# Kernel optimization log

Hardware: AMD Instinct MI355X
Metric: run time of the kernel (lower is better)

## Reference

```python
import jax, jax.numpy as jnp
import numpy as np

INPUT_DIM = 512
KEY_DIM = 256
VOCAB = 10000
MAX_LEN = 300


def setup_inputs() -> dict:
    key = jax.random.key(0)
    ks = jax.random.split(key, 20)
    s = 0.05
    B, S, D, K, V = 32, 196, INPUT_DIM, KEY_DIM, VOCAB
    inp = {
        'x': jax.random.normal(ks[0], (B, S, D), jnp.float32),
        'emb': jax.random.normal(ks[1], (V, D), jnp.float32) * s,
        'Wk': jax.random.normal(ks[2], (K, D), jnp.float32) * s,
        'bk': jnp.zeros((K,), jnp.float32),
        'Wv': jax.random.normal(ks[3], (K, D), jnp.float32) * s,
        'bv': jnp.zeros((K,), jnp.float32),
        'Wq': jax.random.normal(ks[4], (K, D), jnp.float32) * s,
        'bq': jnp.zeros((K,), jnp.float32),
        'Wp': jax.random.normal(ks[5], (V, D + K), jnp.float32) * s,
        'bp': jnp.zeros((V,), jnp.float32),
        # LSTM cell 0: input = concat(embed, context) -> D + K
        'Wih0': jax.random.normal(ks[6], (4 * D, D + K), jnp.float32) * s,
        'Whh0': jax.random.normal(ks[7], (4 * D, D), jnp.float32) * s,
        'bih0': jnp.zeros((4 * D,), jnp.float32),
        'bhh0': jnp.zeros((4 * D,), jnp.float32),
        # LSTM cell 1: input = hidden of cell 0 -> D
        'Wih1': jax.random.normal(ks[8], (4 * D, D), jnp.float32) * s,
        'Whh1': jax.random.normal(ks[9], (4 * D, D), jnp.float32) * s,
        'bih1': jnp.zeros((4 * D,), jnp.float32),
        'bhh1': jnp.zeros((4 * D,), jnp.float32),
    }
    return inp


def _lstm_cell(inp, h, c, Wih, Whh, bih, bhh):
    # torch LSTMCell gate order: i, f, g, o
    gates = inp @ Wih.T + bih + h @ Whh.T + bhh
    i, f, g, o = jnp.split(gates, 4, axis=-1)
    c_new = jax.nn.sigmoid(f) * c + jax.nn.sigmoid(i) * jnp.tanh(g)
    h_new = jax.nn.sigmoid(o) * jnp.tanh(c_new)
    return h_new, c_new


def reference(x, emb, Wk, bk, Wv, bv, Wq, bq, Wp, bp,
              Wih0, Whh0, bih0, bhh0, Wih1, Whh1, bih1, bhh1):
    B = x.shape[0]
    D = Whh0.shape[1]
    K = Wk.shape[0]
    scale = 1.0 / jnp.sqrt(jnp.asarray(K, x.dtype))
    keys = x @ Wk.T + bk      # (B, S, K)
    values = x @ Wv.T + bv    # (B, S, K)

    tok0 = jnp.zeros((B,), jnp.int32)           # argmax of zeros(B,1) == 0
    ctx0 = jnp.zeros((B, K), x.dtype)
    h0 = jnp.zeros((B, D), x.dtype)
    c0 = jnp.zeros((B, D), x.dtype)
    h1 = jnp.zeros((B, D), x.dtype)
    c1 = jnp.zeros((B, D), x.dtype)

    def step(carry, _):
        tok, ctx, h0, c0, h1, c1 = carry
        embed = jnp.concatenate([emb[tok], ctx], axis=1)   # (B, D+K)
        h0, c0 = _lstm_cell(embed, h0, c0, Wih0, Whh0, bih0, bhh0)
        h1, c1 = _lstm_cell(h0, h1, c1, Wih1, Whh1, bih1, bhh1)
        q = h1 @ Wq.T + bq                                  # (B, K)
        energy = jnp.einsum('bsk,bk->bs', keys, q) * scale  # (B, S)
        attn = jax.nn.softmax(energy, axis=-1)
        ctx = jnp.einsum('bs,bsk->bk', attn, values)        # (B, K)
        out = jnp.concatenate([h1, ctx], axis=1)            # (B, D+K)
        pred = out @ Wp.T + bp                              # (B, V)
        tok = jnp.argmax(pred, axis=-1).astype(jnp.int32)
        return (tok, ctx, h0, c0, h1, c1), pred

    _, preds = jax.lax.scan(step, (tok0, ctx0, h0, c0, h1, c1), None, length=MAX_LEN)
    return jnp.transpose(preds, (1, 0, 2))  # (B, MAX_LEN, V)
```

## Files before the change

kernel.cpp:

```cpp
#include <hip/hip_runtime.h>
#include <math.h>


typedef unsigned long long u64;
typedef float v4f __attribute__((ext_vector_type(4)));

#define NS 196
#define ND 512
#define NK 256
#define NV 10000
#define NT 300
#define NBLK 256
#define NTHR 512
#define NPRED 209
#define ATT0 224
#define SCOPE __HIP_MEMORY_SCOPE_AGENT

__device__ __forceinline__ float sigm(float x) { return 1.0f / (1.0f + expf(-x)); }

__device__ __forceinline__ float aldf(const float* p) {
  return __hip_atomic_load(p, __ATOMIC_RELAXED, SCOPE);
}
__device__ __forceinline__ void astf(float* p, float v) {
  __hip_atomic_store(p, v, __ATOMIC_RELAXED, SCOPE);
}
__device__ __forceinline__ u64 aldu(const u64* p) {
  return __hip_atomic_load(p, __ATOMIC_RELAXED, SCOPE);
}
__device__ __forceinline__ void astu(u64* p, u64 v) {
  __hip_atomic_store(p, v, __ATOMIC_RELAXED, SCOPE);
}
__device__ __forceinline__ v4f ald16(const float* p) {
  union { u64 q[2]; v4f v; } u;
  u.q[0] = __hip_atomic_load((const u64*)p + 0, __ATOMIC_RELAXED, SCOPE);
  u.q[1] = __hip_atomic_load((const u64*)p + 1, __ATOMIC_RELAXED, SCOPE);
  return u.v;
}

__device__ __forceinline__ u64 packmax(float x, int v) {
  unsigned u = __float_as_uint(x);
  u = (u & 0x80000000u) ? ~u : (u | 0x80000000u);
  return ((u64)u << 32) | (u64)(0xFFFFFFFFu - (unsigned)v);
}

__device__ __forceinline__ int eslot(int b, int k4) {
  return b * 32 + ((k4 & ~7) | ((k4 ^ b) & 7));
}

__device__ __forceinline__ void gbar(unsigned* bar, int bid, unsigned ep, bool fenced) {
  __syncthreads();
  if (threadIdx.x == 0) {
    if (fenced) __threadfence();
    asm volatile("s_waitcnt vmcnt(0)" ::: "memory");
    const int g = bid & 7;
    const unsigned old = __hip_atomic_fetch_add(&bar[g * 32], 1u, __ATOMIC_RELAXED, SCOPE);
    if (old == ep * 32u - 1u) {
      const unsigned r = __hip_atomic_fetch_add(&bar[512], 1u, __ATOMIC_RELAXED, SCOPE);
      if (r == ep * 8u - 1u) {
#pragma unroll
        for (int i = 0; i < 8; ++i)
          __hip_atomic_store(&bar[256 + i * 32], ep, __ATOMIC_RELAXED, SCOPE);
      }
    }
    while (__hip_atomic_load(&bar[256 + g * 32], __ATOMIC_RELAXED, SCOPE) < ep)
      __builtin_amdgcn_s_sleep(1);
    if (fenced) __threadfence();
  }
  __syncthreads();
}

__global__ __launch_bounds__(256) void k_zbar(unsigned* bar) {
  const int i = blockIdx.x * 256 + threadIdx.x;
  if (i < 1024) bar[i] = 0u;
}

struct Params {
  const float *x, *emb, *Wk, *bk, *Wv, *bv, *Wq, *bq, *Wp, *bp;
  const float *Wih0, *Whh0, *bih0, *bhh0, *Wih1, *Whh1, *bih1, *bhh1;
  float *out, *keys, *values, *h0t, *h1t, *c0, *c1, *ctx;
  u64 *amax;
  unsigned *bar;
};

__global__ __launch_bounds__(NTHR, 1) void k_all(Params p) {
  extern __shared__ float dyn[];
  float* W0lds = dyn;
  float* W1lds = dyn + 10240;
  float* stage = dyn + 18432;

  __shared__ __align__(16) float arena[2560];
  __shared__ int tok_lds[32];
  __shared__ u64 cand2[32][12];

  const int bid = blockIdx.x;
  const int t = threadIdx.x;
  const int lane = t & 63;
  const int w = t >> 6;

  {
    const int g = bid * NTHR + t;
    if (g < 65536) astf(&p.h0t[g], 0.0f);
    if (g < 8192) astf(&p.ctx[g], 0.0f);
    if (g < 256) astu(&p.amax[g], (g < 32) ? ((1ull << 32) | 0xFFFFFFFFull) : 0ull);
  }
  if (t < 64) {
    const int idx = (bid * 2 + (t >> 5)) * 32 + (t & 31);
    p.c0[idx] = 0.0f;
    p.c1[idx] = 0.0f;
  }
  {
    const int r = t >> 6, ln = t & 63;
    const int grow = (r >> 1) * ND + bid * 2 + (r & 1);
    const float* s0i = p.Wih0 + (size_t)grow * 768;
    const float* s0h = p.Whh0 + (size_t)grow * ND;
#pragma unroll
    for (int j = 0; j < 5; ++j) {
      const int col = 4 * (ln + 64 * j);
      const float4 v = (col < 768) ? *(const float4*)(s0i + col)
                                   : *(const float4*)(s0h + (col - 768));
      *(float4*)(W0lds + r * 1280 + col) = v;
    }
    const float* s1i = p.Wih1 + (size_t)grow * ND;
    const float* s1h = p.Whh1 + (size_t)grow * ND;
#pragma unroll
    for (int j = 0; j < 4; ++j) {
      const int col = 4 * (ln + 64 * j);
      const float4 v = (col < 512) ? *(const float4*)(s1i + col)
                                   : *(const float4*)(s1h + (col - 512));
      *(float4*)(W1lds + r * 1024 + col) = v;
    }
  }
  {
    const int kc = bid & 7, bb = bid >> 3;
    const int kl = t & 31, sg = t >> 5;
    const int k = kc * 32 + kl;
    float ak[13], av[13];
#pragma unroll
    for (int i = 0; i < 13; ++i) { ak[i] = 0.f; av[i] = 0.f; }
    const float* wkr = p.Wk + (size_t)k * ND;
    const float* wvr = p.Wv + (size_t)k * ND;
    const float* xb = p.x + (size_t)bb * NS * ND;
    for (int j = 0; j < ND; j += 4) {
      const float4 wk4 = *(const float4*)(wkr + j);
      const float4 wv4 = *(const float4*)(wvr + j);
#pragma unroll
      for (int si = 0; si < 13; ++si) {
        const int s = sg + si * 16;
        if (s < NS) {
          const float4 xv = *(const float4*)(xb + (size_t)s * ND + j);
          ak[si] += wk4.x * xv.x + wk4.y * xv.y + wk4.z * xv.z + wk4.w * xv.w;
          av[si] += wv4.x * xv.x + wv4.y * xv.y + wv4.z * xv.z + wv4.w * xv.w;
        }
      }
    }
    const float bkk = p.bk[k], bvv = p.bv[k];
#pragma unroll
    for (int si = 0; si < 13; ++si) {
      const int s = sg + si * 16;
      if (s < NS) {
        const size_t o = ((size_t)bb * NS + s) * NK + k;
        p.keys[o] = ak[si] + bkk;
        p.values[o] = av[si] + bvv;
      }
    }
  }
  unsigned ep = 1;
  gbar(p.bar, bid, ep++, true);

  for (int step = 0; step < NT; ++step) {
    const int cur = step & 1;
    const float* h0c = p.h0t + cur * 16384;
    float* h0n = p.h0t + (cur ^ 1) * 16384;
    const float* h1c = p.h1t + cur * 16384;
    float* h1n = p.h1t + (cur ^ 1) * 16384;

    if (t < 32) {
      u64 m = aldu(&p.amax[t]);
#pragma unroll
      for (int s2 = 1; s2 < 8; ++s2) { const u64 o = aldu(&p.amax[s2 * 32 + t]); if (o > m) m = o; }
      tok_lds[t] = (int)(0xFFFFFFFFu - (unsigned)(m & 0xFFFFFFFFull));
    }
    __syncthreads();
    {
      const int rq = w >> 2, ks = w & 3;
      const int b = lane & 31, kq = lane >> 5;
      const int rb = rq * 4;
      float a0 = 0.f, a1 = 0.f, a2 = 0.f, a3 = 0.f;
      for (int c = 0; c < 4; ++c) {
        {
          const int eb = t >> 4, sl = t & 15;
          const float* er = p.emb + (size_t)tok_lds[eb] * ND + c * 128;
          *(float4*)(stage + 4 * eslot(eb, sl)) = *(const float4*)(er + 4 * sl);
          *(float4*)(stage + 4 * eslot(eb, sl + 16)) = *(const float4*)(er + 4 * (sl + 16));
        }
        __syncthreads();
#pragma unroll
        for (int jj = 0; jj < 4; ++jj) {
          const int f4 = ks * 8 + kq * 4 + jj;
          const float4 a4 = *(const float4*)(stage + 4 * eslot(b, f4));
          const int wc = c * 128 + 4 * f4;
          const float4 q0 = *(const float4*)(W0lds + (rb + 0) * 1280 + wc);
          const float4 q1 = *(const float4*)(W0lds + (rb + 1) * 1280 + wc);
          const float4 q2 = *(const float4*)(W0lds + (rb + 2) * 1280 + wc);
          const float4 q3 = *(const float4*)(W0lds + (rb + 3) * 1280 + wc);
          a0 += q0.x * a4.x + q0.y * a4.y + q0.z * a4.z + q0.w * a4.w;
          a1 += q1.x * a4.x + q1.y * a4.y + q1.z * a4.z + q1.w * a4.w;
          a2 += q2.x * a4.x + q2.y * a4.y + q2.z * a4.z + q2.w * a4.w;
          a3 += q3.x * a4.x + q3.y * a4.y + q3.z * a4.z + q3.w * a4.w;
        }
        __syncthreads();
      }
      a0 += __shfl_xor(a0, 32);
      a1 += __shfl_xor(a1, 32);
      a2 += __shfl_xor(a2, 32);
      a3 += __shfl_xor(a3, 32);
      if (kq == 0) {
        arena[(ks * 8 + rb + 0) * 32 + b] = a0;
        arena[(ks * 8 + rb + 1) * 32 + b] = a1;
        arena[(ks * 8 + rb + 2) * 32 + b] = a2;
        arena[(ks * 8 + rb + 3) * 32 + b] = a3;
      }
    }
    {
      const int rq4 = w >> 1, kh = w & 1;
      const int bq = lane & 7, kl = lane >> 3;
      const int r0 = rq4 * 2, r1 = r0 + 1;
      const float* wr0 = W0lds + r0 * 1280 + 512 + kh * 384 + kl * 4;
      const float* wr1 = W0lds + r1 * 1280 + 512 + kh * 384 + kl * 4;
      v4f ac0 = {0.f, 0.f, 0.f, 0.f}, ac1 = {0.f, 0.f, 0.f, 0.f};
#pragma unroll 3
      for (int j = 0; j < 12; ++j) {
        const int kk = kh * 384 + j * 32 + kl * 4;
        const float* asrc = (kk < 256) ? (p.ctx + (size_t)kk * 32)
                                       : (h0c + (size_t)(kk - 256) * 32);
        const v4f x0 = ald16(asrc + 0 * 32 + bq * 4);
        const v4f x1 = ald16(asrc + 1 * 32 + bq * 4);
        const v4f x2 = ald16(asrc + 2 * 32 + bq * 4);
        const v4f x3 = ald16(asrc + 3 * 32 + bq * 4);
        const v4f q0 = *(const v4f*)(wr0 + j * 32);
        const v4f q1 = *(const v4f*)(wr1 + j * 32);
        ac0 += q0[0] * x0 + q0[1] * x1 + q0[2] * x2 + q0[3] * x3;
        ac1 += q1[0] * x0 + q1[1] * x1 + q1[2] * x2 + q1[3] * x3;
      }
#pragma unroll
      for (int c = 0; c < 4; ++c) {
        float v0 = ac0[c], v1 = ac1[c];
        v0 += __shfl_xor(v0, 8);  v1 += __shfl_xor(v1, 8);
        v0 += __shfl_xor(v0, 16); v1 += __shfl_xor(v1, 16);
        v0 += __shfl_xor(v0, 32); v1 += __shfl_xor(v1, 32);
        ac0[c] = v0; ac1[c] = v1;
      }
      if (kl == 0) {
#pragma unroll
        for (int i = 0; i < 4; ++i) {
          arena[1024 + (kh * 8 + r0) * 32 + bq * 4 + i] = ac0[i];
          arena[1024 + (kh * 8 + r1) * 32 + bq * 4 + i] = ac1[i];
        }
      }
    }
    __syncthreads();
    if (t < 256) {
      const int r = t >> 5, b2 = t & 31;
      const int grow = (r >> 1) * ND + bid * 2 + (r & 1);
      arena[1536 + r * 32 + b2] =
          arena[(0 * 8 + r) * 32 + b2] + arena[(1 * 8 + r) * 32 + b2]
        + arena[(2 * 8 + r) * 32 + b2] + arena[(3 * 8 + r) * 32 + b2]
        + arena[1024 + (0 * 8 + r) * 32 + b2] + arena[1024 + (1 * 8 + r) * 32 + b2]
        + p.bih0[grow] + p.bhh0[grow];
    }
    __syncthreads();
    if (t < 64) {
      const int dl = t >> 5, b2 = t & 31;
      const int idx = (bid * 2 + dl) * 32 + b2;
      const float gi = arena[1536 + (0 + dl) * 32 + b2], gf = arena[1536 + (2 + dl) * 32 + b2];
      const float gg = arena[1536 + (4 + dl) * 32 + b2], go = arena[1536 + (6 + dl) * 32 + b2];
      const float cn = sigm(gf) * p.c0[idx] + sigm(gi) * tanhf(gg);
      p.c0[idx] = cn;
      astf(&h0n[idx], sigm(go) * tanhf(cn));
    }
    gbar(p.bar, bid, ep++, false);

    if (bid == 0 && t < 256) astu(&p.amax[t], 0ull);
    {
      const int rq4 = w >> 1, kh = w & 1;
      const int bq = lane & 7, kl = lane >> 3;
      const int r0 = rq4 * 2, r1 = r0 + 1;
      const float* wr0 = W1lds + r0 * 1024 + kh * 512 + kl * 4;
      const float* wr1 = W1lds + r1 * 1024 + kh * 512 + kl * 4;
      const float* abase = (kh == 0) ? h0n : h1c;
      v4f ac0 = {0.f, 0.f, 0.f, 0.f}, ac1 = {0.f, 0.f, 0.f, 0.f};
#pragma unroll 4
      for (int j = 0; j < 16; ++j) {
        const float* asrc = abase + (size_t)(j * 32 + kl * 4) * 32;
        const v4f x0 = ald16(asrc + 0 * 32 + bq * 4);
        const v4f x1 = ald16(asrc + 1 * 32 + bq * 4);
        const v4f x2 = ald16(asrc + 2 * 32 + bq * 4);
        const v4f x3 = ald16(asrc + 3 * 32 + bq * 4);
        const v4f q0 = *(const v4f*)(wr0 + j * 32);
        const v4f q1 = *(const v4f*)(wr1 + j * 32);
        ac0 += q0[0] * x0 + q0[1] * x1 + q0[2] * x2 + q0[3] * x3;
        ac1 += q1[0] * x0 + q1[1] * x1 + q1[2] * x2 + q1[3] * x3;
      }
#pragma unroll
      for (int c = 0; c < 4; ++c) {
        float v0 = ac0[c], v1 = ac1[c];
        v0 += __shfl_xor(v0, 8);  v1 += __shfl_xor(v1, 8);
        v0 += __shfl_xor(v0, 16); v1 += __shfl_xor(v1, 16);
        v0 += __shfl_xor(v0, 32); v1 += __shfl_xor(v1, 32);
        ac0[c] = v0; ac1[c] = v1;
      }
      if (kl == 0) {
#pragma unroll
        for (int i = 0; i < 4; ++i) {
          arena[(kh * 8 + r0) * 32 + bq * 4 + i] = ac0[i];
          arena[(kh * 8 + r1) * 32 + bq * 4 + i] = ac1[i];
        }
      }
    }
    __syncthreads();
    if (t < 256) {
      const int r = t >> 5, b2 = t & 31;
      const int grow = (r >> 1) * ND + bid * 2 + (r & 1);
      arena[512 + r * 32 + b2] =
          arena[(0 * 8 + r) * 32 + b2] + arena[(1 * 8 + r) * 32 + b2]
        + p.bih1[grow] + p.bhh1[grow];
    }
    __syncthreads();
    if (t < 64) {
      const int dl = t >> 5, b2 = t & 31;
      const int idx = (bid * 2 + dl) * 32 + b2;
      const float gi = arena[512 + (0 + dl) * 32 + b2], gf = arena[512 + (2 + dl) * 32 + b2];
      const float gg = arena[512 + (4 + dl) * 32 + b2], go = arena[512 + (6 + dl) * 32 + b2];
      const float cn = sigm(gf) * p.c1[idx] + sigm(gi) * tanhf(gg);
      p.c1[idx] = cn;
      astf(&h1n[idx], sigm(go) * tanhf(cn));
    }
    gbar(p.bar, bid, ep++, false);

    v4f pa[6];
#pragma unroll
    for (int r = 0; r < 6; ++r) pa[r] = (v4f){0.f, 0.f, 0.f, 0.f};
    if (bid >= ATT0) {
      const int b = bid - ATT0;
      float* hb  = arena;
      float* qs  = arena + 512;
      float* red = arena + 768;
      float* smx = arena + 1024;
      hb[t] = aldf(h1n + t * 32 + b);
      __syncthreads();
      const int kl = lane & 31, rh = lane >> 5;
      for (int pp = 0; pp < 16; ++pp) {
        const int r = w * 32 + pp * 2 + rh;
        const float* wq = p.Wq + (size_t)r * ND + kl * 4;
        float a = 0.f;
#pragma unroll
        for (int i = 0; i < 4; ++i) {
          const float4 w4 = *(const float4*)(wq + i * 128);
          const float4 h4 = *(const float4*)(hb + i * 128 + kl * 4);
          a += w4.x * h4.x + w4.y * h4.y + w4.z * h4.z + w4.w * h4.w;
        }
#pragma unroll
        for (int mk = 1; mk < 32; mk <<= 1) a += __shfl_xor(a, mk);
        if (kl == 0) qs[r] = (a + p.bq[r]) * 0.0625f;
      }
      __syncthreads();
      for (int pp = 0; pp < 13; ++pp) {
        const int s = pp * 16 + w * 2 + rh;
        float a = 0.f;
        if (s < NS) {
          const float* kr = p.keys + ((size_t)b * NS + s) * NK + kl * 4;
#pragma unroll
          for (int i = 0; i < 2; ++i) {
            const float4 k4 = *(const float4*)(kr + i * 128);
            const float4 q4 = *(const float4*)(qs + i * 128 + kl * 4);
            a += k4.x * q4.x + k4.y * q4.y + k4.z * q4.z + k4.w * q4.w;
          }
        }
#pragma unroll
        for (int mk = 1; mk < 32; mk <<= 1) a += __shfl_xor(a, mk);
        if (kl == 0 && s < NS) smx[s] = a;
      }
      __syncthreads();
      float e = -INFINITY;
      if (t < 256) { e = (t < NS) ? smx[t] : -INFINITY; red[t] = e; }
      __syncthreads();
      for (int off = 128; off; off >>= 1) {
        if (t < off) red[t] = fmaxf(red[t], red[t + off]);
        __syncthreads();
      }
      const float mx = red[0];
      __syncthreads();
      float a = 0.f;
      if (t < 256) { a = (t < NS) ? expf(e - mx) : 0.f; red[t] = a; }
      __syncthreads();
      for (int off = 128; off; off >>= 1) {
        if (t < off) red[t] += red[t + off];
        __syncthreads();
      }
      const float inv = 1.0f / red[0];
      if (t < 256) smx[t] = a * inv;
      __syncthreads();
      if (t < 256) {
        const float* vb = p.values + (size_t)b * NS * NK + t;
        float c0_ = 0.f, c1_ = 0.f, c2_ = 0.f, c3_ = 0.f;
        for (int s = 0; s < NS; s += 4) {
          c0_ += smx[s + 0] * vb[(size_t)(s + 0) * NK];
          c1_ += smx[s + 1] * vb[(size_t)(s + 1) * NK];
          c2_ += smx[s + 2] * vb[(size_t)(s + 2) * NK];
          c3_ += smx[s + 3] * vb[(size_t)(s + 3) * NK];
        }
        astf(&p.ctx[t * 32 + b], (c0_ + c1_) + (c2_ + c3_));
      }
    } else if (bid < NPRED) {
      const int bq = lane & 7, kl = lane >> 3;
      const int rbase = bid * 48 + w * 6;
      int rc[6];
#pragma unroll
      for (int r = 0; r < 6; ++r) rc[r] = (rbase + r < NV) ? (rbase + r) : (NV - 1);
#pragma unroll 2
      for (int j = 0; j < 16; ++j) {
        const int kk = j * 32 + kl * 4;
        const float* asrc = h1n + (size_t)kk * 32;
        const v4f x0 = ald16(asrc + 0 * 32 + bq * 4);
        const v4f x1 = ald16(asrc + 1 * 32 + bq * 4);
        const v4f x2 = ald16(asrc + 2 * 32 + bq * 4);
        const v4f x3 = ald16(asrc + 3 * 32 + bq * 4);
#pragma unroll
        for (int r = 0; r < 6; ++r) {
          const v4f q = *(const v4f*)(p.Wp + (size_t)rc[r] * 768 + kk);
          pa[r] += q[0] * x0 + q[1] * x1 + q[2] * x2 + q[3] * x3;
        }
      }
    }
    gbar(p.bar, bid, ep++, false);

    if (bid < NPRED) {
      const int bq = lane & 7, kl = lane >> 3;
      const int rbase = bid * 48 + w * 6;
      int rc[6];
#pragma unroll
      for (int r = 0; r < 6; ++r) rc[r] = (rbase + r < NV) ? (rbase + r) : (NV - 1);
#pragma unroll 2
      for (int j = 0; j < 8; ++j) {
        const int kk = j * 32 + kl * 4;
        const float* asrc = p.ctx + (size_t)kk * 32;
        const v4f x0 = ald16(asrc + 0 * 32 + bq * 4);
        const v4f x1 = ald16(asrc + 1 * 32 + bq * 4);
        const v4f x2 = ald16(asrc + 2 * 32 + bq * 4);
        const v4f x3 = ald16(asrc + 3 * 32 + bq * 4);
#pragma unroll
        for (int r = 0; r < 6; ++r) {
          const v4f q = *(const v4f*)(p.Wp + (size_t)rc[r] * 768 + 512 + kk);
          pa[r] += q[0] * x0 + q[1] * x1 + q[2] * x2 + q[3] * x3;
        }
      }
#pragma unroll
      for (int r = 0; r < 6; ++r) {
#pragma unroll
        for (int c = 0; c < 4; ++c) {
          float v = pa[r][c];
          v += __shfl_xor(v, 8);
          v += __shfl_xor(v, 16);
          v += __shfl_xor(v, 32);
          pa[r][c] = v;
        }
      }
      if (kl == 0) {
#pragma unroll
        for (int r = 0; r < 6; ++r)
#pragma unroll
          for (int i = 0; i < 4; ++i)
            arena[(w * 6 + r) * 32 + bq * 4 + i] = pa[r][i];
      }
      __syncthreads();
      if (t < 384) {
        const int b2 = t & 31, rg = t >> 5;
        const int vb = bid * 48 + rg * 4;
        u64 m = 0ull;
        if (vb + 3 < NV) {
          float4 v;
          float* vp = &v.x;
#pragma unroll
          for (int i = 0; i < 4; ++i) {
            const int row = rg * 4 + i;
            vp[i] = arena[row * 32 + b2] + p.bp[vb + i];
          }
          *(float4*)(p.out + ((size_t)b2 * NT + step) * NV + vb) = v;
          m = packmax(v.x, vb + 0);
          const u64 o1 = packmax(v.y, vb + 1); if (o1 > m) m = o1;
          const u64 o2 = packmax(v.z, vb + 2); if (o2 > m) m = o2;
          const u64 o3 = packmax(v.w, vb + 3); if (o3 > m) m = o3;
        }
        cand2[b2][rg] = m;
      }
      __syncthreads();
      if (t < 32) {
        u64 mm = cand2[t][0];
#pragma unroll
        for (int i = 1; i < 12; ++i) { const u64 o = cand2[t][i]; if (o > mm) mm = o; }
        (void)__hip_atomic_fetch_max(&p.amax[(bid & 7) * 32 + t], mm, __ATOMIC_RELAXED, SCOPE);
      }
    }
    gbar(p.bar, bid, ep++, false);
  }
}

extern "C" void kernel_launch(void* const* d_in, const int* in_sizes, int n_in,
                              void* d_out, int out_size, void* d_ws, size_t ws_size,
                              hipStream_t stream) {
  (void)in_sizes; (void)n_in; (void)out_size; (void)ws_size;
  Params prm;
  prm.x    = (const float*)d_in[0];
  prm.emb  = (const float*)d_in[1];
  prm.Wk   = (const float*)d_in[2];
  prm.bk   = (const float*)d_in[3];
  prm.Wv   = (const float*)d_in[4];
  prm.bv   = (const float*)d_in[5];
  prm.Wq   = (const float*)d_in[6];
  prm.bq   = (const float*)d_in[7];
  prm.Wp   = (const float*)d_in[8];
  prm.bp   = (const float*)d_in[9];
  prm.Wih0 = (const float*)d_in[10];
  prm.Whh0 = (const float*)d_in[11];
  prm.bih0 = (const float*)d_in[12];
  prm.bhh0 = (const float*)d_in[13];
  prm.Wih1 = (const float*)d_in[14];
  prm.Whh1 = (const float*)d_in[15];
  prm.bih1 = (const float*)d_in[16];
  prm.bhh1 = (const float*)d_in[17];
  prm.out  = (float*)d_out;

  float* ws = (float*)d_ws;
  prm.keys   = ws;
  prm.values = prm.keys + 1605632;
  prm.h0t    = prm.values + 1605632;
  prm.h1t    = prm.h0t + 32768;
  prm.c0     = prm.h1t + 32768;
  prm.c1     = prm.c0 + 16384;
  prm.ctx    = prm.c1 + 16384;
  prm.amax   = (u64*)(prm.ctx + 8192);
  prm.bar    = (unsigned*)(prm.amax + 256);

  const int LDS = (10240 + 8192 + 4096) * 4;
  (void)hipFuncSetAttribute((const void*)k_all, hipFuncAttributeMaxDynamicSharedMemorySize, LDS);

  k_zbar<<<4, 256, 0, stream>>>(prm.bar);
  void* args[] = { &prm };
  (void)hipLaunchCooperativeKernel((const void*)k_all, dim3(NBLK), dim3(NTHR), args,
                                   (unsigned)LDS, stream);
}
```

Measured before the change: 24.68 ms.

## Replace hierarchical atomic-counter grid barrier with flag-based checker-block barrier

```diff
diff --git a/kernel.cpp b/kernel.cpp
--- a/kernel.cpp
+++ b/kernel.cpp
@@ -14,6 +14,7 @@
 #define NTHR 512
 #define NPRED 209
 #define ATT0 224
+#define CHECKER 223
 #define SCOPE __HIP_MEMORY_SCOPE_AGENT
 
 __device__ __forceinline__ float sigm(float x) { return 1.0f / (1.0f + expf(-x)); }
@@ -28,6 +29,12 @@
   return __hip_atomic_load(p, __ATOMIC_RELAXED, SCOPE);
 }
 __device__ __forceinline__ void astu(u64* p, u64 v) {
+  __hip_atomic_store(p, v, __ATOMIC_RELAXED, SCOPE);
+}
+__device__ __forceinline__ unsigned ald32(const unsigned* p) {
+  return __hip_atomic_load(p, __ATOMIC_RELAXED, SCOPE);
+}
+__device__ __forceinline__ void ast32(unsigned* p, unsigned v) {
   __hip_atomic_store(p, v, __ATOMIC_RELAXED, SCOPE);
 }
 __device__ __forceinline__ v4f ald16(const float* p) {
@@ -44,34 +51,35 @@
 }
 
 __device__ __forceinline__ int eslot(int b, int k4) {
-  return b * 32 + ((k4 & ~7) | ((k4 ^ b) & 7));
+  return b * 64 + ((k4 & ~7) | ((k4 ^ b) & 7));
 }
 
 __device__ __forceinline__ void gbar(unsigned* bar, int bid, unsigned ep, bool fenced) {
   __syncthreads();
-  if (threadIdx.x == 0) {
+  const int t = threadIdx.x;
+  if (t == 0) {
     if (fenced) __threadfence();
     asm volatile("s_waitcnt vmcnt(0)" ::: "memory");
-    const int g = bid & 7;
-    const unsigned old = __hip_atomic_fetch_add(&bar[g * 32], 1u, __ATOMIC_RELAXED, SCOPE);
-    if (old == ep * 32u - 1u) {
-      const unsigned r = __hip_atomic_fetch_add(&bar[512], 1u, __ATOMIC_RELAXED, SCOPE);
-      if (r == ep * 8u - 1u) {
-#pragma unroll
-        for (int i = 0; i < 8; ++i)
-          __hip_atomic_store(&bar[256 + i * 32], ep, __ATOMIC_RELAXED, SCOPE);
-      }
-    }
-    while (__hip_atomic_load(&bar[256 + g * 32], __ATOMIC_RELAXED, SCOPE) < ep)
-      __builtin_amdgcn_s_sleep(1);
-    if (fenced) __threadfence();
+    ast32(&bar[bid * 4], ep);
+  }
+  if (bid == CHECKER) {
+    if (t < 256) {
+      while (ald32(&bar[t * 4]) < ep) __builtin_amdgcn_s_sleep(1);
+    }
+    __syncthreads();
+    if (t < 256) ast32(&bar[1024 + t * 4], ep);
+  } else {
+    if (t == 0) {
+      while (ald32(&bar[1024 + bid * 4]) < ep) __builtin_amdgcn_s_sleep(1);
+      if (fenced) __threadfence();
+    }
   }
   __syncthreads();
 }
 
 __global__ __launch_bounds__(256) void k_zbar(unsigned* bar) {
   const int i = blockIdx.x * 256 + threadIdx.x;
-  if (i < 1024) bar[i] = 0u;
+  if (i < 2048) bar[i] = 0u;
 }
 
 struct Params {
@@ -101,7 +109,7 @@
     const int g = bid * NTHR + t;
     if (g < 65536) astf(&p.h0t[g], 0.0f);
     if (g < 8192) astf(&p.ctx[g], 0.0f);
-    if (g < 256) astu(&p.amax[g], (g < 32) ? ((1ull << 32) | 0xFFFFFFFFull) : 0ull);
+    if (g < 1024) astu(&p.amax[g], (g < 32) ? ((1ull << 32) | 0xFFFFFFFFull) : 0ull);
   }
   if (t < 64) {
     const int idx = (bid * 2 + (t >> 5)) * 32 + (t & 31);
@@ -177,7 +185,7 @@
     if (t < 32) {
       u64 m = aldu(&p.amax[t]);
 #pragma unroll
-      for (int s2 = 1; s2 < 8; ++s2) { const u64 o = aldu(&p.amax[s2 * 32 + t]); if (o > m) m = o; }
+      for (int s2 = 1; s2 < 32; ++s2) { const u64 o = aldu(&p.amax[s2 * 32 + t]); if (o > m) m = o; }
       tok_lds[t] = (int)(0xFFFFFFFFu - (unsigned)(m & 0xFFFFFFFFull));
     }
     __syncthreads();
@@ -186,19 +194,22 @@
       const int b = lane & 31, kq = lane >> 5;
       const int rb = rq * 4;
       float a0 = 0.f, a1 = 0.f, a2 = 0.f, a3 = 0.f;
-      for (int c = 0; c < 4; ++c) {
+      for (int c = 0; c < 2; ++c) {
         {
           const int eb = t >> 4, sl = t & 15;
-          const float* er = p.emb + (size_t)tok_lds[eb] * ND + c * 128;
-          *(float4*)(stage + 4 * eslot(eb, sl)) = *(const float4*)(er + 4 * sl);
-          *(float4*)(stage + 4 * eslot(eb, sl + 16)) = *(const float4*)(er + 4 * (sl + 16));
+          const float* er = p.emb + (size_t)tok_lds[eb] * ND + c * 256;
+#pragma unroll
+          for (int u = 0; u < 4; ++u) {
+            const int k4c = sl + u * 16;
+            *(float4*)(stage + 4 * eslot(eb, k4c)) = *(const float4*)(er + 4 * k4c);
+          }
         }
         __syncthreads();
 #pragma unroll
-        for (int jj = 0; jj < 4; ++jj) {
-          const int f4 = ks * 8 + kq * 4 + jj;
+        for (int jj = 0; jj < 8; ++jj) {
+          const int f4 = ks * 16 + kq * 8 + jj;
           const float4 a4 = *(const float4*)(stage + 4 * eslot(b, f4));
-          const int wc = c * 128 + 4 * f4;
+          const int wc = c * 256 + 4 * f4;
           const float4 q0 = *(const float4*)(W0lds + (rb + 0) * 1280 + wc);
           const float4 q1 = *(const float4*)(W0lds + (rb + 1) * 1280 + wc);
           const float4 q2 = *(const float4*)(W0lds + (rb + 2) * 1280 + wc);
@@ -280,7 +291,7 @@
     }
     gbar(p.bar, bid, ep++, false);
 
-    if (bid == 0 && t < 256) astu(&p.amax[t], 0ull);
+    if (bid == 0) { astu(&p.amax[t], 0ull); astu(&p.amax[512 + t], 0ull); }
     {
       const int rq4 = w >> 1, kh = w & 1;
       const int bq = lane & 7, kl = lane >> 3;
@@ -498,7 +509,7 @@
         u64 mm = cand2[t][0];
 #pragma unroll
         for (int i = 1; i < 12; ++i) { const u64 o = cand2[t][i]; if (o > mm) mm = o; }
-        (void)__hip_atomic_fetch_max(&p.amax[(bid & 7) * 32 + t], mm, __ATOMIC_RELAXED, SCOPE);
+        (void)__hip_atomic_fetch_max(&p.amax[(bid & 31) * 32 + t], mm, __ATOMIC_RELAXED, SCOPE);
       }
     }
     gbar(p.bar, bid, ep++, false);
@@ -539,12 +550,12 @@
   prm.c1     = prm.c0 + 16384;
   prm.ctx    = prm.c1 + 16384;
   prm.amax   = (u64*)(prm.ctx + 8192);
-  prm.bar    = (unsigned*)(prm.amax + 256);
-
-  const int LDS = (10240 + 8192 + 4096) * 4;
+  prm.bar    = (unsigned*)(prm.amax + 1024);
+
+  const int LDS = (10240 + 8192 + 8192) * 4;
   (void)hipFuncSetAttribute((const void*)k_all, hipFuncAttributeMaxDynamicSharedMemorySize, LDS);
 
-  k_zbar<<<4, 256, 0, stream>>>(prm.bar);
+  k_zbar<<<8, 256, 0, stream>>>(prm.bar);
   void* args[] = { &prm };
   (void)hipLaunchCooperativeKernel((const void*)k_all, dim3(NBLK), dim3(NTHR), args,
                                    (unsigned)LDS, stream);
```

After: 26.84 ms. +8.7%, slower.
